# Optimization experiments

Hardware: AMD Instinct MI355X
Metric: run time of the kernel (lower is better)

## Reference

```python
import jax, jax.numpy as jnp
import numpy as np

DECAY = 0.95

def setup_inputs() -> dict:
    key = jax.random.key(0)
    k1, k2, k3, k4 = jax.random.split(key, 4)
    B, S, H, Dk, Dv = 4, 4096, 16, 64, 64
    return {
        "memory": jax.random.normal(k1, (H, Dk, Dv), dtype=jnp.float32),
        "keys": jax.random.normal(k2, (B, S, H, Dk), dtype=jnp.float32),
        "values": jax.random.normal(k3, (B, S, H, Dv), dtype=jnp.float32),
        "write_strengths": jax.random.uniform(k4, (B, S), dtype=jnp.float32),
    }

def reference(memory, keys, values, write_strengths):
    # M_new = decay * M + sum_{b,s} rho[b,s] * k[b,s,h] v[b,s,h]^T
    # Algebraically equivalent to per-head (rho-weighted) K^T V contraction;
    # avoids materializing the (B,S,H,Dk,Dv) outer-product tensor.
    delta = jnp.einsum('bs,bshk,bshv->hkv', write_strengths, keys, values)
    return DECAY * memory + delta
```

## Files before the change

### kernel.cpp

```cpp
#include <hip/hip_runtime.h>


constexpr int HH = 16;
constexpr int DK = 64;
constexpr int DV = 64;
constexpr int ROWS = 16384;
constexpr int NCHUNK = 64;
constexpr int RPB = ROWS / NCHUNK;
constexpr int RPW = RPB / 4;
constexpr int TR = 8;
constexpr int NT = RPW / TR;
constexpr float DECAY = 0.95f;

__global__ __launch_bounds__(256) void init_out(const float* __restrict__ mem,
                                                float* __restrict__ out) {
    int i = blockIdx.x * 256 + threadIdx.x;
    out[i] = DECAY * mem[i];
}

__global__ __launch_bounds__(256, 4) void accum(const float* __restrict__ keys,
                                                const float* __restrict__ values,
                                                const float* __restrict__ rho,
                                                float* __restrict__ out) {
    __shared__ float smem[8192];

    const int t    = threadIdx.x;
    const int w    = t >> 6;
    const int lane = t & 63;
    const int tk   = lane >> 3;
    const int tv   = lane & 7;
    const int chunk = blockIdx.x;
    const int h     = blockIdx.y;

    float* kb = smem + w * 1024;
    float* vb = smem + 4096 + w * 1024;

    const int row0 = chunk * RPB + w * RPW;
    const int sr = lane >> 4;
    const int sc = (lane & 15) * 4;

    float acc[8][8];
    #pragma unroll
    for (int i = 0; i < 8; ++i)
        #pragma unroll
        for (int j = 0; j < 8; ++j) acc[i][j] = 0.f;

    float4 kr0, kr1, vr0, vr1;
    float w0, w1;

    {
        int r = row0;
        const float* kp = keys   + ((r + sr) * HH + h) * DK + sc;
        const float* vp = values + ((r + sr) * HH + h) * DV + sc;
        kr0 = *(const float4*)kp;
        kr1 = *(const float4*)(kp + 4 * HH * DK);
        vr0 = *(const float4*)vp;
        vr1 = *(const float4*)(vp + 4 * HH * DV);
        w0 = rho[r + sr];
        w1 = rho[r + sr + 4];
        kr0.x *= w0; kr0.y *= w0; kr0.z *= w0; kr0.w *= w0;
        kr1.x *= w1; kr1.y *= w1; kr1.z *= w1; kr1.w *= w1;
        *(float4*)(kb + lane * 4)       = kr0;
        *(float4*)(kb + 256 + lane * 4) = kr1;
        *(float4*)(vb + lane * 4)       = vr0;
        *(float4*)(vb + 256 + lane * 4) = vr1;
    }

    for (int tile = 0; tile < NT; ++tile) {
        const int cur = tile & 1;
        const int nxt = cur ^ 1;
        const bool more = (tile + 1) < NT;

        if (more) {
            int r = row0 + (tile + 1) * TR;
            const float* kp = keys   + ((r + sr) * HH + h) * DK + sc;
            const float* vp = values + ((r + sr) * HH + h) * DV + sc;
            kr0 = *(const float4*)kp;
            kr1 = *(const float4*)(kp + 4 * HH * DK);
            vr0 = *(const float4*)vp;
            vr1 = *(const float4*)(vp + 4 * HH * DV);
            w0 = rho[r + sr];
            w1 = rho[r + sr + 4];
        }

        const float* kc = kb + cur * 512;
        const float* vc = vb + cur * 512;
        #pragma unroll
        for (int s = 0; s < TR; ++s) {
            float4 ka  = *(const float4*)(kc + s * 64 + tk * 8);
            float4 ka2 = *(const float4*)(kc + s * 64 + tk * 8 + 4);
            float4 va  = *(const float4*)(vc + s * 64 + tv * 8);
            float4 va2 = *(const float4*)(vc + s * 64 + tv * 8 + 4);
            float kv[8] = {ka.x, ka.y, ka.z, ka.w, ka2.x, ka2.y, ka2.z, ka2.w};
            float vv[8] = {va.x, va.y, va.z, va.w, va2.x, va2.y, va2.z, va2.w};
            #pragma unroll
            for (int i = 0; i < 8; ++i)
                #pragma unroll
                for (int j = 0; j < 8; ++j)
                    acc[i][j] = fmaf(kv[i], vv[j], acc[i][j]);
        }

        if (more) {
            kr0.x *= w0; kr0.y *= w0; kr0.z *= w0; kr0.w *= w0;
            kr1.x *= w1; kr1.y *= w1; kr1.z *= w1; kr1.w *= w1;
            float* kn = kb + nxt * 512;
            float* vn = vb + nxt * 512;
            *(float4*)(kn + lane * 4)       = kr0;
            *(float4*)(kn + 256 + lane * 4) = kr1;
            *(float4*)(vn + lane * 4)       = vr0;
            *(float4*)(vn + 256 + lane * 4) = vr1;
        }
    }

    __syncthreads();
    float* red0 = smem;
    float* red1 = smem + 4096;

    if (w < 2) {
        float* dst = (w == 0) ? red0 : red1;
        #pragma unroll
        for (int i = 0; i < 8; ++i) {
            float4 a0 = {acc[i][0], acc[i][1], acc[i][2], acc[i][3]};
            float4 a1 = {acc[i][4], acc[i][5], acc[i][6], acc[i][7]};
            *(float4*)(dst + (tk * 8 + i) * 64 + tv * 8)     = a0;
            *(float4*)(dst + (tk * 8 + i) * 64 + tv * 8 + 4) = a1;
        }
    }
    __syncthreads();
    if (w >= 2) {
        float* dst = (w == 2) ? red0 : red1;
        #pragma unroll
        for (int i = 0; i < 8; ++i) {
            float4* p0 = (float4*)(dst + (tk * 8 + i) * 64 + tv * 8);
            float4* p1 = p0 + 1;
            float4 c0 = *p0, c1 = *p1;
            c0.x += acc[i][0]; c0.y += acc[i][1]; c0.z += acc[i][2]; c0.w += acc[i][3];
            c1.x += acc[i][4]; c1.y += acc[i][5]; c1.z += acc[i][6]; c1.w += acc[i][7];
            *p0 = c0; *p1 = c1;
        }
    }
    __syncthreads();

    float* o = out + h * (DK * DV);
    #pragma unroll
    for (int i = 0; i < 16; ++i) {
        int idx = i * 256 + t;
        atomicAdd(o + idx, red0[idx] + red1[idx]);
    }
}

extern "C" void kernel_launch(void* const* d_in, const int* in_sizes, int n_in,
                              void* d_out, int out_size, void* d_ws, size_t ws_size,
                              hipStream_t stream) {
    const float* mem    = (const float*)d_in[0];
    const float* keys   = (const float*)d_in[1];
    const float* values = (const float*)d_in[2];
    const float* rho    = (const float*)d_in[3];
    float* out = (float*)d_out;

    init_out<<<dim3((HH * DK * DV) / 256), dim3(256), 0, stream>>>(mem, out);

    dim3 grid(NCHUNK, HH);
    accum<<<grid, dim3(256), 0, stream>>>(keys, values, rho, out);
}
```

Before: 168.2 us.

## Stage K/V tiles into LDS with direct global-to-LDS loads shared across waves

Replaces per-wave register-staged loads with `global_load_lds` DMA that fills block-wide 32-row K and V tiles, double-buffered, with one barrier per tile. The write strengths are staged once into LDS and applied to the keys at compute time instead of before the LDS store. The aim is to cut VGPR staging and load/store instructions and improve memory-level parallelism on this bandwidth-bound contraction. The trade-offs are extra block-wide barriers per tile and dropping the occupancy hint from launch_bounds, and correctness depends on the compiler waiting for the async LDS writes before each barrier.

```diff
diff --git a/kernel.cpp b/kernel.cpp
--- a/kernel.cpp
+++ b/kernel.cpp
@@ -7,9 +7,8 @@
 constexpr int ROWS = 16384;
 constexpr int NCHUNK = 64;
 constexpr int RPB = ROWS / NCHUNK;
-constexpr int RPW = RPB / 4;
-constexpr int TR = 8;
-constexpr int NT = RPW / TR;
+constexpr int TSR = 32;
+constexpr int NT = RPB / TSR;
 constexpr float DECAY = 0.95f;
 
 __global__ __launch_bounds__(256) void init_out(const float* __restrict__ mem,
@@ -18,11 +17,19 @@
     out[i] = DECAY * mem[i];
 }
 
-__global__ __launch_bounds__(256, 4) void accum(const float* __restrict__ keys,
-                                                const float* __restrict__ values,
-                                                const float* __restrict__ rho,
-                                                float* __restrict__ out) {
-    __shared__ float smem[8192];
+__device__ __forceinline__ void dma16(const float* g, float* l) {
+    __builtin_amdgcn_global_load_lds(
+        (const __attribute__((address_space(1))) void*)g,
+        (__attribute__((address_space(3))) void*)l, 16, 0, 0);
+}
+
+__global__ __launch_bounds__(256) void accum(const float* __restrict__ keys,
+                                             const float* __restrict__ values,
+                                             const float* __restrict__ rho,
+                                             float* __restrict__ out) {
+    __shared__ float sK[2][TSR * DK];
+    __shared__ float sV[2][TSR * DV];
+    __shared__ float sR[RPB];
 
     const int t    = threadIdx.x;
     const int w    = t >> 6;
@@ -31,121 +38,110 @@
     const int tv   = lane & 7;
     const int chunk = blockIdx.x;
     const int h     = blockIdx.y;
+    const int row0  = chunk * RPB;
 
-    float* kb = smem + w * 1024;
-    float* vb = smem + 4096 + w * 1024;
+    const int dr = t >> 4;
+    const int dc = (t & 15) * 4;
 
-    const int row0 = chunk * RPB + w * RPW;
-    const int sr = lane >> 4;
-    const int sc = (lane & 15) * 4;
-
-    float acc[8][8];
-    #pragma unroll
-    for (int i = 0; i < 8; ++i)
-        #pragma unroll
-        for (int j = 0; j < 8; ++j) acc[i][j] = 0.f;
-
-    float4 kr0, kr1, vr0, vr1;
-    float w0, w1;
+    __builtin_amdgcn_global_load_lds(
+        (const __attribute__((address_space(1))) void*)(rho + row0 + t),
+        (__attribute__((address_space(3))) void*)(sR + t), 4, 0, 0);
 
     {
-        int r = row0;
-        const float* kp = keys   + ((r + sr) * HH + h) * DK + sc;
-        const float* vp = values + ((r + sr) * HH + h) * DV + sc;
-        kr0 = *(const float4*)kp;
-        kr1 = *(const float4*)(kp + 4 * HH * DK);
-        vr0 = *(const float4*)vp;
-        vr1 = *(const float4*)(vp + 4 * HH * DV);
-        w0 = rho[r + sr];
-        w1 = rho[r + sr + 4];
-        kr0.x *= w0; kr0.y *= w0; kr0.z *= w0; kr0.w *= w0;
-        kr1.x *= w1; kr1.y *= w1; kr1.z *= w1; kr1.w *= w1;
-        *(float4*)(kb + lane * 4)       = kr0;
-        *(float4*)(kb + 256 + lane * 4) = kr1;
-        *(float4*)(vb + lane * 4)       = vr0;
-        *(float4*)(vb + 256 + lane * 4) = vr1;
+        const float* kg = keys   + ((size_t)(row0 + dr) * HH + h) * DK + dc;
+        const float* vg = values + ((size_t)(row0 + dr) * HH + h) * DV + dc;
+        dma16(kg, &sK[0][dr * DK + dc]);
+        dma16(kg + 16 * HH * DK, &sK[0][(dr + 16) * DK + dc]);
+        dma16(vg, &sV[0][dr * DV + dc]);
+        dma16(vg + 16 * HH * DV, &sV[0][(dr + 16) * DV + dc]);
     }
+
+    float4 acc[8][2];
+    #pragma unroll
+    for (int i = 0; i < 8; ++i) {
+        acc[i][0] = make_float4(0.f, 0.f, 0.f, 0.f);
+        acc[i][1] = make_float4(0.f, 0.f, 0.f, 0.f);
+    }
+
+    __syncthreads();
 
     for (int tile = 0; tile < NT; ++tile) {
         const int cur = tile & 1;
         const int nxt = cur ^ 1;
-        const bool more = (tile + 1) < NT;
 
-        if (more) {
-            int r = row0 + (tile + 1) * TR;
-            const float* kp = keys   + ((r + sr) * HH + h) * DK + sc;
-            const float* vp = values + ((r + sr) * HH + h) * DV + sc;
-            kr0 = *(const float4*)kp;
-            kr1 = *(const float4*)(kp + 4 * HH * DK);
-            vr0 = *(const float4*)vp;
-            vr1 = *(const float4*)(vp + 4 * HH * DV);
-            w0 = rho[r + sr];
-            w1 = rho[r + sr + 4];
+        if (tile + 1 < NT) {
+            const int r = row0 + (tile + 1) * TSR + dr;
+            const float* kg = keys   + ((size_t)r * HH + h) * DK + dc;
+            const float* vg = values + ((size_t)r * HH + h) * DV + dc;
+            dma16(kg, &sK[nxt][dr * DK + dc]);
+            dma16(kg + 16 * HH * DK, &sK[nxt][(dr + 16) * DK + dc]);
+            dma16(vg, &sV[nxt][dr * DV + dc]);
+            dma16(vg + 16 * HH * DV, &sV[nxt][(dr + 16) * DV + dc]);
         }
 
-        const float* kc = kb + cur * 512;
-        const float* vc = vb + cur * 512;
+        const float* kb = &sK[cur][w * 8 * DK];
+        const float* vb = &sV[cur][w * 8 * DV];
+        const float* rb = &sR[tile * TSR + w * 8];
+
         #pragma unroll
-        for (int s = 0; s < TR; ++s) {
-            float4 ka  = *(const float4*)(kc + s * 64 + tk * 8);
-            float4 ka2 = *(const float4*)(kc + s * 64 + tk * 8 + 4);
-            float4 va  = *(const float4*)(vc + s * 64 + tv * 8);
-            float4 va2 = *(const float4*)(vc + s * 64 + tv * 8 + 4);
-            float kv[8] = {ka.x, ka.y, ka.z, ka.w, ka2.x, ka2.y, ka2.z, ka2.w};
-            float vv[8] = {va.x, va.y, va.z, va.w, va2.x, va2.y, va2.z, va2.w};
-            #pragma unroll
-            for (int i = 0; i < 8; ++i)
-                #pragma unroll
-                for (int j = 0; j < 8; ++j)
-                    acc[i][j] = fmaf(kv[i], vv[j], acc[i][j]);
+        for (int si = 0; si < 8; ++si) {
+            float4 kf  = *(const float4*)(kb + si * DK + tk * 8);
+            float4 kf2 = *(const float4*)(kb + si * DK + tk * 8 + 4);
+            float4 vf  = *(const float4*)(vb + si * DV + tv * 8);
+            float4 vf2 = *(const float4*)(vb + si * DV + tv * 8 + 4);
+            float r = rb[si];
+            kf.x *= r; kf.y *= r; kf.z *= r; kf.w *= r;
+            kf2.x *= r; kf2.y *= r; kf2.z *= r; kf2.w *= r;
+
+            #define FMA_ROW(I, KV)                                  \
+                acc[I][0].x = fmaf(KV, vf.x,  acc[I][0].x);         \
+                acc[I][0].y = fmaf(KV, vf.y,  acc[I][0].y);         \
+                acc[I][0].z = fmaf(KV, vf.z,  acc[I][0].z);         \
+                acc[I][0].w = fmaf(KV, vf.w,  acc[I][0].w);         \
+                acc[I][1].x = fmaf(KV, vf2.x, acc[I][1].x);         \
+                acc[I][1].y = fmaf(KV, vf2.y, acc[I][1].y);         \
+                acc[I][1].z = fmaf(KV, vf2.z, acc[I][1].z);         \
+                acc[I][1].w = fmaf(KV, vf2.w, acc[I][1].w);
+            FMA_ROW(0, kf.x)  FMA_ROW(1, kf.y)  FMA_ROW(2, kf.z)  FMA_ROW(3, kf.w)
+            FMA_ROW(4, kf2.x) FMA_ROW(5, kf2.y) FMA_ROW(6, kf2.z) FMA_ROW(7, kf2.w)
+            #undef FMA_ROW
         }
 
-        if (more) {
-            kr0.x *= w0; kr0.y *= w0; kr0.z *= w0; kr0.w *= w0;
-            kr1.x *= w1; kr1.y *= w1; kr1.z *= w1; kr1.w *= w1;
-            float* kn = kb + nxt * 512;
-            float* vn = vb + nxt * 512;
-            *(float4*)(kn + lane * 4)       = kr0;
-            *(float4*)(kn + 256 + lane * 4) = kr1;
-            *(float4*)(vn + lane * 4)       = vr0;
-            *(float4*)(vn + 256 + lane * 4) = vr1;
-        }
+        __syncthreads();
     }
 
-    __syncthreads();
-    float* red0 = smem;
-    float* red1 = smem + 4096;
+    float* red = (w & 1) ? &sV[0][0] : &sK[0][0];
 
     if (w < 2) {
-        float* dst = (w == 0) ? red0 : red1;
         #pragma unroll
         for (int i = 0; i < 8; ++i) {
-            float4 a0 = {acc[i][0], acc[i][1], acc[i][2], acc[i][3]};
-            float4 a1 = {acc[i][4], acc[i][5], acc[i][6], acc[i][7]};
-            *(float4*)(dst + (tk * 8 + i) * 64 + tv * 8)     = a0;
-            *(float4*)(dst + (tk * 8 + i) * 64 + tv * 8 + 4) = a1;
+            *(float4*)(red + (tk * 8 + i) * 64 + tv * 8)     = acc[i][0];
+            *(float4*)(red + (tk * 8 + i) * 64 + tv * 8 + 4) = acc[i][1];
         }
     }
     __syncthreads();
     if (w >= 2) {
-        float* dst = (w == 2) ? red0 : red1;
         #pragma unroll
         for (int i = 0; i < 8; ++i) {
-            float4* p0 = (float4*)(dst + (tk * 8 + i) * 64 + tv * 8);
+            float4* p0 = (float4*)(red + (tk * 8 + i) * 64 + tv * 8);
             float4* p1 = p0 + 1;
             float4 c0 = *p0, c1 = *p1;
-            c0.x += acc[i][0]; c0.y += acc[i][1]; c0.z += acc[i][2]; c0.w += acc[i][3];
-            c1.x += acc[i][4]; c1.y += acc[i][5]; c1.z += acc[i][6]; c1.w += acc[i][7];
+            c0.x += acc[i][0].x; c0.y += acc[i][0].y;
+            c0.z += acc[i][0].z; c0.w += acc[i][0].w;
+            c1.x += acc[i][1].x; c1.y += acc[i][1].y;
+            c1.z += acc[i][1].z; c1.w += acc[i][1].w;
             *p0 = c0; *p1 = c1;
         }
     }
     __syncthreads();
 
     float* o = out + h * (DK * DV);
+    const float* r0 = &sK[0][0];
+    const float* r1 = &sV[0][0];
     #pragma unroll
     for (int i = 0; i < 16; ++i) {
         int idx = i * 256 + t;
-        atomicAdd(o + idx, red0[idx] + red1[idx]);
+        atomicAdd(o + idx, r0[idx] + r1[idx]);
     }
 }
 
```

Result: no change. 165.9 us (-1.3%).
